# Optimization experiments

Hardware: AMD Instinct MI355X
Metric: run time of the kernel (lower is better)

Reference implementation:

```python
import jax, jax.numpy as jnp
import numpy as np

C_EMB = 64  # n_embd


def setup_inputs() -> dict:
    key = jax.random.key(0)
    ks = jax.random.split(key, 7)
    B, T, C, H, BS = 2, 512, C_EMB, 64, 512
    s = lambda k, shp, sc: (jax.random.normal(k, shp, dtype=jnp.float32) * sc)
    return {
        "x": s(ks[0], (B, T, C), 1.0),
        "pos_table": s(ks[1], (BS, C), 0.02),
        "W1": s(ks[2], (C, 4 * C), (4 * C) ** -0.5),  # Linear(4C -> C), torch layout [out,in]
        "b1": s(ks[3], (C,), 0.01),
        "W2": s(ks[4], (1, C), C ** -0.5),            # Linear(C -> 1)
        "b2": s(ks[5], (1,), 0.01),
        "Wv": s(ks[6], (H, C), C ** -0.5),            # Linear(C -> H, bias=False)
    }


def reference(x, pos_table, W1, b1, W2, b2, Wv):
    B, T, C = x.shape
    # x1 = cat([pos_emb, x], -1): [B,T,2C]
    pos = pos_table[:T]  # [T,C]
    x1 = jnp.concatenate([jnp.broadcast_to(pos[None], (B, T, C)), x], axis=-1)  # [B,T,2C]
    # a2[b,i,j] = cat([x1[b,j], x1[b,i]]); Linear(4C->C) splits into key/query halves.
    Wk = W1[:, : 2 * C]   # acts on x1_j
    Wq = W1[:, 2 * C :]   # acts on x1_i
    hk = jnp.einsum('btd,cd->btc', x1, Wk)  # [B,T,C] indexed by j
    hq = jnp.einsum('btd,cd->btc', x1, Wq)  # [B,T,C] indexed by i
    hidden = jax.nn.relu(hq[:, :, None, :] + hk[:, None, :, :] + b1)  # [B,T(i),T(j),C]
    scores = jnp.einsum('bijc,c->bij', hidden, W2[0]) + b2[0]          # [B,T,T]
    wei = scores * (C ** -0.5)
    causal = jnp.tril(jnp.ones((T, T), dtype=bool))
    wei = jnp.where(causal[None], wei, -jnp.inf)
    wei = jax.nn.softmax(wei, axis=-1)  # dropout p=0 -> identity
    v = jnp.einsum('btc,hc->bth', x, Wv)  # [B,T,H]
    return jnp.einsum('bij,bjh->bih', wei, v)
```

## Files before the change

kernel.cpp:

```cpp
#include <hip/hip_runtime.h>
#include <math.h>

constexpr int TLEN = 512;
constexpr int CDIM = 64;
constexpr int BDIM = 2;

__global__ __launch_bounds__(256) void proj_kernel(
    const float* __restrict__ x, const float* __restrict__ pos,
    const float* __restrict__ W1, const float* __restrict__ b1,
    float4* __restrict__ hkt4, float* __restrict__ hqb)
{
    const int tid = threadIdx.x;
    const int r0g = blockIdx.x * 4;
    const int b   = r0g >> 9;
    const int t0  = r0g & (TLEN - 1);

    __shared__ float4 w1_s[64 * 64];
    __shared__ alignas(16) float x1s[4][128];
    __shared__ float hks[CDIM][5];

    const float4* W1f4 = (const float4*)W1;
    #pragma unroll
    for (int m = tid; m < 64 * 64; m += 256) {
        const int c = m >> 6, e4 = m & 63;
        w1_s[c * 64 + (e4 ^ (c & 63))] = W1f4[c * 64 + e4];
    }
    #pragma unroll
    for (int e = tid; e < 4 * 128; e += 256) {
        const int r4 = e >> 7, d = e & 127;
        const int grow = r0g + r4;
        const int tt = grow & (TLEN - 1);
        x1s[r4][d] = (d < CDIM) ? pos[tt * CDIM + d]
                                : x[grow * CDIM + (d - CDIM)];
    }
    __syncthreads();

    {
        const int sub = tid >> 6, c = tid & 63;
        const int grow = r0g + sub;
        const float4* xv = (const float4*)x1s[sub];
        const float4* wb = w1_s + c * 64;
        const int sw = c & 63;
        float4 ak = make_float4(0.f, 0.f, 0.f, 0.f);
        float4 aq = ak;
        #pragma unroll
        for (int d4 = 0; d4 < 32; ++d4) {
            const float4 xx = xv[d4];
            const float4 wk = wb[d4 ^ sw];
            const float4 wq = wb[(32 + d4) ^ sw];
            ak.x = fmaf(xx.x, wk.x, ak.x); ak.y = fmaf(xx.y, wk.y, ak.y);
            ak.z = fmaf(xx.z, wk.z, ak.z); ak.w = fmaf(xx.w, wk.w, ak.w);
            aq.x = fmaf(xx.x, wq.x, aq.x); aq.y = fmaf(xx.y, wq.y, aq.y);
            aq.z = fmaf(xx.z, wq.z, aq.z); aq.w = fmaf(xx.w, wq.w, aq.w);
        }
        hks[c][sub] = (ak.x + ak.y) + (ak.z + ak.w);
        hqb[grow * CDIM + c] = (aq.x + aq.y) + (aq.z + aq.w) + b1[c];
    }
    __syncthreads();

    if (tid < 64) {
        const int c4 = tid >> 2, tl = tid & 3;
        const float4 v = make_float4(hks[c4 * 4 + 0][tl], hks[c4 * 4 + 1][tl],
                                     hks[c4 * 4 + 2][tl], hks[c4 * 4 + 3][tl]);
        hkt4[(b * 16 + c4) * TLEN + t0 + tl] = v;
    }
}

__global__ __launch_bounds__(512, 4) void attn_kernel(
    const float* __restrict__ x,   const float* __restrict__ W2,
    const float* __restrict__ b2,  const float* __restrict__ Wv,
    const float4* __restrict__ hkt4, const float4* __restrict__ hqb4,
    float* __restrict__ out)
{
    const int tid = threadIdx.x;
    const int idx = blockIdx.x;
    const int b   = idx & 1;
    const int p   = idx >> 1;
    int rr[2];
    rr[0] = p; rr[1] = (TLEN - 1) - p;

    __shared__ float4 wv_s[64 * 16];
    __shared__ float4 hq_s[2][16];
    __shared__ float4 w24_s[16];
    __shared__ alignas(16) float pS[2][TLEN];
    __shared__ float2 wreds[8];
    __shared__ float pvs[2][8][CDIM];
    __shared__ alignas(16) float o_s[2][CDIM];

    const float4* Wvf4 = (const float4*)Wv;
    #pragma unroll
    for (int m = tid; m < 64 * 16; m += 512) {
        const int hh = m >> 4, e4 = m & 15;
        wv_s[hh * 16 + (e4 ^ (hh & 15))] = Wvf4[hh * 16 + e4];
    }
    if (tid < 32) {
        const int rp = tid >> 4, e = tid & 15;
        hq_s[rp][e] = hqb4[(b * TLEN + rr[rp]) * 16 + e];
    } else if (tid < 48) {
        w24_s[tid - 32] = ((const float4*)W2)[tid - 32];
    }
    __syncthreads();

    const float b2v = b2[0];
    const float4* hk4b = hkt4 + b * 16 * TLEN;
    const int j = tid;
    const int w = tid >> 6;
    const bool act0 = ((w << 6) <= rr[0]);

    float4 acc0 = make_float4(0.f, 0.f, 0.f, 0.f);
    float4 acc1 = acc0;
    if (act0) {
        #pragma unroll
        for (int c4 = 0; c4 < 16; ++c4) {
            const float4 kk = hk4b[c4 * TLEN + j];
            const float4 q0 = hq_s[0][c4];
            const float4 q1 = hq_s[1][c4];
            const float4 ww = w24_s[c4];
            acc0.x = fmaf(fmaxf(kk.x + q0.x, 0.f), ww.x, acc0.x);
            acc0.y = fmaf(fmaxf(kk.y + q0.y, 0.f), ww.y, acc0.y);
            acc0.z = fmaf(fmaxf(kk.z + q0.z, 0.f), ww.z, acc0.z);
            acc0.w = fmaf(fmaxf(kk.w + q0.w, 0.f), ww.w, acc0.w);
            acc1.x = fmaf(fmaxf(kk.x + q1.x, 0.f), ww.x, acc1.x);
            acc1.y = fmaf(fmaxf(kk.y + q1.y, 0.f), ww.y, acc1.y);
            acc1.z = fmaf(fmaxf(kk.z + q1.z, 0.f), ww.z, acc1.z);
            acc1.w = fmaf(fmaxf(kk.w + q1.w, 0.f), ww.w, acc1.w);
        }
    } else {
        #pragma unroll
        for (int c4 = 0; c4 < 16; ++c4) {
            const float4 kk = hk4b[c4 * TLEN + j];
            const float4 q1 = hq_s[1][c4];
            const float4 ww = w24_s[c4];
            acc1.x = fmaf(fmaxf(kk.x + q1.x, 0.f), ww.x, acc1.x);
            acc1.y = fmaf(fmaxf(kk.y + q1.y, 0.f), ww.y, acc1.y);
            acc1.z = fmaf(fmaxf(kk.z + q1.z, 0.f), ww.z, acc1.z);
            acc1.w = fmaf(fmaxf(kk.w + q1.w, 0.f), ww.w, acc1.w);
        }
    }

    float sw0 = 0.f, sw1;
    if (act0) {
        const float sv = ((acc0.x + acc0.y) + (acc0.z + acc0.w) + b2v) * 0.125f;
        const float pt = (j <= rr[0]) ? __expf(sv) : 0.f;
        pS[0][j] = pt;
        float sm = pt;
        #pragma unroll
        for (int off = 32; off > 0; off >>= 1)
            sm += __shfl_xor(sm, off);
        sw0 = sm;
    }
    {
        const float sv = ((acc1.x + acc1.y) + (acc1.z + acc1.w) + b2v) * 0.125f;
        const float pt = (j <= rr[1]) ? __expf(sv) : 0.f;
        pS[1][j] = pt;
        float sm = pt;
        #pragma unroll
        for (int off = 32; off > 0; off >>= 1)
            sm += __shfl_xor(sm, off);
        sw1 = sm;
    }
    if ((tid & 63) == 0) wreds[w] = make_float2(sw0, sw1);
    __syncthreads();

    const int h = tid & 63;
    const int g = w;
    const float* xh = x + b * TLEN * CDIM + h;
    const int nj4 = (rr[1] >> 2) + 1;
    float4 a0 = make_float4(0.f, 0.f, 0.f, 0.f);
    float4 a1 = a0;
    for (int j4 = g; j4 < nj4; j4 += 8) {
        const int j0 = j4 * 4;
        const float4 p1v = ((const float4*)pS[1])[j4];
        const float x0 = xh[j0 * CDIM];
        const float x1 = xh[(j0 + 1) * CDIM];
        const float x2 = xh[(j0 + 2) * CDIM];
        const float x3 = xh[(j0 + 3) * CDIM];
        a1.x = fmaf(p1v.x, x0, a1.x); a1.y = fmaf(p1v.y, x1, a1.y);
        a1.z = fmaf(p1v.z, x2, a1.z); a1.w = fmaf(p1v.w, x3, a1.w);
        if (j0 <= rr[0]) {
            const float4 p0v = ((const float4*)pS[0])[j4];
            a0.x = fmaf(p0v.x, x0, a0.x); a0.y = fmaf(p0v.y, x1, a0.y);
            a0.z = fmaf(p0v.z, x2, a0.z); a0.w = fmaf(p0v.w, x3, a0.w);
        }
    }
    pvs[0][g][h] = (a0.x + a0.y) + (a0.z + a0.w);
    pvs[1][g][h] = (a1.x + a1.y) + (a1.z + a1.w);
    __syncthreads();
    if (tid < 128) {
        const int k = tid >> 6, hh = tid & 63;
        float o = pvs[k][0][hh];
        #pragma unroll
        for (int ww = 1; ww < 8; ++ww) o += pvs[k][ww][hh];
        float gsum = 0.f;
        #pragma unroll
        for (int ww = 0; ww < 8; ++ww)
            gsum += (k == 0) ? wreds[ww].x : wreds[ww].y;
        o_s[k][hh] = o / gsum;
    }
    __syncthreads();
    if (tid < 128) {
        const int k = tid >> 6, hh = tid & 63;
        const float4* wb = wv_s + hh * 16;
        const int sw = hh & 15;
        const float4* o4 = (const float4*)o_s[k];
        float4 a = make_float4(0.f, 0.f, 0.f, 0.f);
        #pragma unroll
        for (int c4 = 0; c4 < 16; ++c4) {
            const float4 wwv = wb[c4 ^ sw];
            const float4 oo = o4[c4];
            a.x = fmaf(oo.x, wwv.x, a.x); a.y = fmaf(oo.y, wwv.y, a.y);
            a.z = fmaf(oo.z, wwv.z, a.z); a.w = fmaf(oo.w, wwv.w, a.w);
        }
        out[(b * TLEN + rr[k]) * CDIM + hh] = (a.x + a.y) + (a.z + a.w);
    }
}

extern "C" void kernel_launch(void* const* d_in, const int* in_sizes, int n_in,
                              void* d_out, int out_size, void* d_ws, size_t ws_size,
                              hipStream_t stream)
{
    const float* x   = (const float*)d_in[0];
    const float* pos = (const float*)d_in[1];
    const float* W1  = (const float*)d_in[2];
    const float* b1  = (const float*)d_in[3];
    const float* W2  = (const float*)d_in[4];
    const float* b2  = (const float*)d_in[5];
    const float* Wv  = (const float*)d_in[6];
    float* out = (float*)d_out;

    float4* hkt4 = (float4*)d_ws;
    float*  hqb  = (float*)d_ws + 4 * 16384;

    proj_kernel<<<BDIM * TLEN / 4, 256, 0, stream>>>(x, pos, W1, b1, hkt4, hqb);
    attn_kernel<<<BDIM * TLEN / 2, 512, 0, stream>>>(x, W2, b2, Wv,
                                                     hkt4, (const float4*)hqb,
                                                     out);
}
```

Measured before the change: 23.09 us.

## Process four query rows per attention block to reuse key loads

```diff
diff --git a/kernel.cpp b/kernel.cpp
--- a/kernel.cpp
+++ b/kernel.cpp
@@ -76,16 +76,16 @@
     const int idx = blockIdx.x;
     const int b   = idx & 1;
     const int p   = idx >> 1;
-    int rr[2];
-    rr[0] = p; rr[1] = (TLEN - 1) - p;
+    int r[4];
+    r[0] = p; r[1] = p + 128; r[2] = 383 - p; r[3] = 511 - p;
 
     __shared__ float4 wv_s[64 * 16];
-    __shared__ float4 hq_s[2][16];
+    __shared__ float4 hq_s[4][16];
     __shared__ float4 w24_s[16];
-    __shared__ alignas(16) float pS[2][TLEN];
-    __shared__ float2 wreds[8];
-    __shared__ float pvs[2][8][CDIM];
-    __shared__ alignas(16) float o_s[2][CDIM];
+    __shared__ alignas(16) float pS[4][TLEN];
+    __shared__ float4 wreds4[8];
+    __shared__ float pvs[4][8][CDIM];
+    __shared__ alignas(16) float o_s[4][CDIM];
 
     const float4* Wvf4 = (const float4*)Wv;
     #pragma unroll
@@ -93,11 +93,11 @@
         const int hh = m >> 4, e4 = m & 15;
         wv_s[hh * 16 + (e4 ^ (hh & 15))] = Wvf4[hh * 16 + e4];
     }
-    if (tid < 32) {
-        const int rp = tid >> 4, e = tid & 15;
-        hq_s[rp][e] = hqb4[(b * TLEN + rr[rp]) * 16 + e];
-    } else if (tid < 48) {
-        w24_s[tid - 32] = ((const float4*)W2)[tid - 32];
+    if (tid < 64) {
+        const int l = tid >> 4, e = tid & 15;
+        hq_s[l][e] = hqb4[(b * TLEN + r[l]) * 16 + e];
+    } else if (tid < 80) {
+        w24_s[tid - 64] = ((const float4*)W2)[tid - 64];
     }
     __syncthreads();
 
@@ -105,104 +105,111 @@
     const float4* hk4b = hkt4 + b * 16 * TLEN;
     const int j = tid;
     const int w = tid >> 6;
-    const bool act0 = ((w << 6) <= rr[0]);
 
     float4 acc0 = make_float4(0.f, 0.f, 0.f, 0.f);
-    float4 acc1 = acc0;
-    if (act0) {
-        #pragma unroll
-        for (int c4 = 0; c4 < 16; ++c4) {
-            const float4 kk = hk4b[c4 * TLEN + j];
-            const float4 q0 = hq_s[0][c4];
-            const float4 q1 = hq_s[1][c4];
-            const float4 ww = w24_s[c4];
-            acc0.x = fmaf(fmaxf(kk.x + q0.x, 0.f), ww.x, acc0.x);
-            acc0.y = fmaf(fmaxf(kk.y + q0.y, 0.f), ww.y, acc0.y);
-            acc0.z = fmaf(fmaxf(kk.z + q0.z, 0.f), ww.z, acc0.z);
-            acc0.w = fmaf(fmaxf(kk.w + q0.w, 0.f), ww.w, acc0.w);
-            acc1.x = fmaf(fmaxf(kk.x + q1.x, 0.f), ww.x, acc1.x);
-            acc1.y = fmaf(fmaxf(kk.y + q1.y, 0.f), ww.y, acc1.y);
-            acc1.z = fmaf(fmaxf(kk.z + q1.z, 0.f), ww.z, acc1.z);
-            acc1.w = fmaf(fmaxf(kk.w + q1.w, 0.f), ww.w, acc1.w);
-        }
-    } else {
-        #pragma unroll
-        for (int c4 = 0; c4 < 16; ++c4) {
-            const float4 kk = hk4b[c4 * TLEN + j];
-            const float4 q1 = hq_s[1][c4];
-            const float4 ww = w24_s[c4];
-            acc1.x = fmaf(fmaxf(kk.x + q1.x, 0.f), ww.x, acc1.x);
-            acc1.y = fmaf(fmaxf(kk.y + q1.y, 0.f), ww.y, acc1.y);
-            acc1.z = fmaf(fmaxf(kk.z + q1.z, 0.f), ww.z, acc1.z);
-            acc1.w = fmaf(fmaxf(kk.w + q1.w, 0.f), ww.w, acc1.w);
-        }
-    }
-
-    float sw0 = 0.f, sw1;
-    if (act0) {
-        const float sv = ((acc0.x + acc0.y) + (acc0.z + acc0.w) + b2v) * 0.125f;
-        const float pt = (j <= rr[0]) ? __expf(sv) : 0.f;
-        pS[0][j] = pt;
+    float4 acc1 = acc0, acc2 = acc0, acc3 = acc0;
+    #pragma unroll
+    for (int c4 = 0; c4 < 16; ++c4) {
+        const float4 kk = hk4b[c4 * TLEN + j];
+        const float4 ww = w24_s[c4];
+        const float4 q0 = hq_s[0][c4];
+        const float4 q1 = hq_s[1][c4];
+        const float4 q2 = hq_s[2][c4];
+        const float4 q3 = hq_s[3][c4];
+        acc0.x = fmaf(fmaxf(kk.x + q0.x, 0.f), ww.x, acc0.x);
+        acc0.y = fmaf(fmaxf(kk.y + q0.y, 0.f), ww.y, acc0.y);
+        acc0.z = fmaf(fmaxf(kk.z + q0.z, 0.f), ww.z, acc0.z);
+        acc0.w = fmaf(fmaxf(kk.w + q0.w, 0.f), ww.w, acc0.w);
+        acc1.x = fmaf(fmaxf(kk.x + q1.x, 0.f), ww.x, acc1.x);
+        acc1.y = fmaf(fmaxf(kk.y + q1.y, 0.f), ww.y, acc1.y);
+        acc1.z = fmaf(fmaxf(kk.z + q1.z, 0.f), ww.z, acc1.z);
+        acc1.w = fmaf(fmaxf(kk.w + q1.w, 0.f), ww.w, acc1.w);
+        acc2.x = fmaf(fmaxf(kk.x + q2.x, 0.f), ww.x, acc2.x);
+        acc2.y = fmaf(fmaxf(kk.y + q2.y, 0.f), ww.y, acc2.y);
+        acc2.z = fmaf(fmaxf(kk.z + q2.z, 0.f), ww.z, acc2.z);
+        acc2.w = fmaf(fmaxf(kk.w + q2.w, 0.f), ww.w, acc2.w);
+        acc3.x = fmaf(fmaxf(kk.x + q3.x, 0.f), ww.x, acc3.x);
+        acc3.y = fmaf(fmaxf(kk.y + q3.y, 0.f), ww.y, acc3.y);
+        acc3.z = fmaf(fmaxf(kk.z + q3.z, 0.f), ww.z, acc3.z);
+        acc3.w = fmaf(fmaxf(kk.w + q3.w, 0.f), ww.w, acc3.w);
+    }
+    float s[4];
+    s[0] = (acc0.x + acc0.y) + (acc0.z + acc0.w);
+    s[1] = (acc1.x + acc1.y) + (acc1.z + acc1.w);
+    s[2] = (acc2.x + acc2.y) + (acc2.z + acc2.w);
+    s[3] = (acc3.x + acc3.y) + (acc3.z + acc3.w);
+
+    float sw4[4];
+    #pragma unroll
+    for (int k = 0; k < 4; ++k) {
+        const float sv = (s[k] + b2v) * 0.125f;
+        const float pt = (j <= r[k]) ? __expf(sv) : 0.f;
+        pS[k][j] = pt;
         float sm = pt;
         #pragma unroll
         for (int off = 32; off > 0; off >>= 1)
             sm += __shfl_xor(sm, off);
-        sw0 = sm;
-    }
-    {
-        const float sv = ((acc1.x + acc1.y) + (acc1.z + acc1.w) + b2v) * 0.125f;
-        const float pt = (j <= rr[1]) ? __expf(sv) : 0.f;
-        pS[1][j] = pt;
-        float sm = pt;
-        #pragma unroll
-        for (int off = 32; off > 0; off >>= 1)
-            sm += __shfl_xor(sm, off);
-        sw1 = sm;
-    }
-    if ((tid & 63) == 0) wreds[w] = make_float2(sw0, sw1);
+        sw4[k] = sm;
+    }
+    if ((tid & 63) == 0)
+        wreds4[w] = make_float4(sw4[0], sw4[1], sw4[2], sw4[3]);
     __syncthreads();
 
     const int h = tid & 63;
     const int g = w;
     const float* xh = x + b * TLEN * CDIM + h;
-    const int nj4 = (rr[1] >> 2) + 1;
+    const int nj4 = (r[3] >> 2) + 1;
     float4 a0 = make_float4(0.f, 0.f, 0.f, 0.f);
-    float4 a1 = a0;
+    float4 a1 = a0, a2 = a0, a3 = a0;
     for (int j4 = g; j4 < nj4; j4 += 8) {
         const int j0 = j4 * 4;
-        const float4 p1v = ((const float4*)pS[1])[j4];
+        const float4 p3v = ((const float4*)pS[3])[j4];
         const float x0 = xh[j0 * CDIM];
         const float x1 = xh[(j0 + 1) * CDIM];
         const float x2 = xh[(j0 + 2) * CDIM];
         const float x3 = xh[(j0 + 3) * CDIM];
-        a1.x = fmaf(p1v.x, x0, a1.x); a1.y = fmaf(p1v.y, x1, a1.y);
-        a1.z = fmaf(p1v.z, x2, a1.z); a1.w = fmaf(p1v.w, x3, a1.w);
-        if (j0 <= rr[0]) {
-            const float4 p0v = ((const float4*)pS[0])[j4];
-            a0.x = fmaf(p0v.x, x0, a0.x); a0.y = fmaf(p0v.y, x1, a0.y);
-            a0.z = fmaf(p0v.z, x2, a0.z); a0.w = fmaf(p0v.w, x3, a0.w);
+        a3.x = fmaf(p3v.x, x0, a3.x); a3.y = fmaf(p3v.y, x1, a3.y);
+        a3.z = fmaf(p3v.z, x2, a3.z); a3.w = fmaf(p3v.w, x3, a3.w);
+        if (j0 <= r[2]) {
+            const float4 pv = ((const float4*)pS[2])[j4];
+            a2.x = fmaf(pv.x, x0, a2.x); a2.y = fmaf(pv.y, x1, a2.y);
+            a2.z = fmaf(pv.z, x2, a2.z); a2.w = fmaf(pv.w, x3, a2.w);
+        }
+        if (j0 <= r[1]) {
+            const float4 pv = ((const float4*)pS[1])[j4];
+            a1.x = fmaf(pv.x, x0, a1.x); a1.y = fmaf(pv.y, x1, a1.y);
+            a1.z = fmaf(pv.z, x2, a1.z); a1.w = fmaf(pv.w, x3, a1.w);
+        }
+        if (j0 <= r[0]) {
+            const float4 pv = ((const float4*)pS[0])[j4];
+            a0.x = fmaf(pv.x, x0, a0.x); a0.y = fmaf(pv.y, x1, a0.y);
+            a0.z = fmaf(pv.z, x2, a0.z); a0.w = fmaf(pv.w, x3, a0.w);
         }
     }
     pvs[0][g][h] = (a0.x + a0.y) + (a0.z + a0.w);
     pvs[1][g][h] = (a1.x + a1.y) + (a1.z + a1.w);
-    __syncthreads();
-    if (tid < 128) {
-        const int k = tid >> 6, hh = tid & 63;
-        float o = pvs[k][0][hh];
-        #pragma unroll
-        for (int ww = 1; ww < 8; ++ww) o += pvs[k][ww][hh];
+    pvs[2][g][h] = (a2.x + a2.y) + (a2.z + a2.w);
+    pvs[3][g][h] = (a3.x + a3.y) + (a3.z + a3.w);
+    __syncthreads();
+    if (tid < 256) {
+        const int l = tid >> 6, hh = tid & 63;
+        float o = pvs[l][0][hh];
+        #pragma unroll
+        for (int ww = 1; ww < 8; ++ww) o += pvs[l][ww][hh];
         float gsum = 0.f;
         #pragma unroll
-        for (int ww = 0; ww < 8; ++ww)
-            gsum += (k == 0) ? wreds[ww].x : wreds[ww].y;
-        o_s[k][hh] = o / gsum;
-    }
-    __syncthreads();
-    if (tid < 128) {
-        const int k = tid >> 6, hh = tid & 63;
+        for (int ww = 0; ww < 8; ++ww) {
+            const float4 rs = wreds4[ww];
+            gsum += (l == 0) ? rs.x : (l == 1) ? rs.y : (l == 2) ? rs.z : rs.w;
+        }
+        o_s[l][hh] = o / gsum;
+    }
+    __syncthreads();
+    if (tid < 256) {
+        const int l = tid >> 6, hh = tid & 63;
         const float4* wb = wv_s + hh * 16;
         const int sw = hh & 15;
-        const float4* o4 = (const float4*)o_s[k];
+        const float4* o4 = (const float4*)o_s[l];
         float4 a = make_float4(0.f, 0.f, 0.f, 0.f);
         #pragma unroll
         for (int c4 = 0; c4 < 16; ++c4) {
@@ -211,7 +218,7 @@
             a.x = fmaf(oo.x, wwv.x, a.x); a.y = fmaf(oo.y, wwv.y, a.y);
             a.z = fmaf(oo.z, wwv.z, a.z); a.w = fmaf(oo.w, wwv.w, a.w);
         }
-        out[(b * TLEN + rr[k]) * CDIM + hh] = (a.x + a.y) + (a.z + a.w);
+        out[(b * TLEN + r[l]) * CDIM + hh] = (a.x + a.y) + (a.z + a.w);
     }
 }
 
@@ -232,7 +239,7 @@
     float*  hqb  = (float*)d_ws + 4 * 16384;
 
     proj_kernel<<<BDIM * TLEN / 4, 256, 0, stream>>>(x, pos, W1, b1, hkt4, hqb);
-    attn_kernel<<<BDIM * TLEN / 2, 512, 0, stream>>>(x, W2, b2, Wv,
+    attn_kernel<<<BDIM * TLEN / 4, 512, 0, stream>>>(x, W2, b2, Wv,
                                                      hkt4, (const float4*)hqb,
                                                      out);
 }
```

Result: slower. 41.36 us (+79.1%).
